# Optimization experiments

Hardware: AMD Instinct MI355X
Metric: run time of the kernel (lower is better)

The kernel has to match this reference:

```python
import jax, jax.numpy as jnp
import numpy as np

B, S = 32768, 512  # rays, max bright spots (= 2*max_samples)


def setup_inputs() -> dict:
    key = jax.random.key(0)
    k1, k2, k3, k4, k5 = jax.random.split(key, 5)
    V = jax.random.normal(k1, (B, 3), dtype=jnp.float32)
    N = jax.random.normal(k2, (B, 3), dtype=jnp.float32)
    N = N / jnp.linalg.norm(N, axis=-1, keepdims=True)
    spots = jax.random.normal(k3, (S, 3), dtype=jnp.float32)
    spots = spots / jnp.linalg.norm(spots, axis=-1, keepdims=True)
    # prefix masks: num_ele[i] <= num_ray[i] <= S (matches kernel's start_ind-j indexing)
    num_ray = jax.random.randint(k4, (B,), S // 2, S + 1)
    num_ele = jax.random.randint(k5, (B,), 0, S // 2)
    j = jnp.arange(S)
    ray_mask = j[None, :] < num_ray[:, None]
    bright_mask = j[None, :] < num_ele[:, None]
    std = jnp.float32(0.05)  # pix_size
    return {"V": V, "N": N, "spots": spots, "ray_mask": ray_mask,
            "bright_mask": bright_mask, "std": std}


def reference(V, N, spots, ray_mask, bright_mask, std):
    Bn, Sn = bright_mask.shape
    # wp.randf(seed): uniform in [0,1), one per written component -> (B,S,3)
    u = jax.random.uniform(jax.random.key(42), (Bn, Sn, 3), dtype=spots.dtype)
    num_ele = bright_mask.sum(axis=1)            # n per row
    num_ray = ray_mask.sum(axis=1)               # start_ind = num_ray - 1
    j = jnp.arange(Sn)
    active = j[None, :] < num_ele[:, None]       # j in range(n)
    jit = spots[None, :, :] + std * u            # jittered light dirs (B,S,3)
    LdotN = jnp.einsum('bsd,bd->bs', jit, N)
    cond = active & (LdotN > 0.0)                # rejection test
    t = num_ray[:, None] - 1 - j[None, :]        # reversed write index
    t_safe = jnp.where(cond & (t >= 0) & (t < Sn), t, Sn)  # Sn -> dropped
    b_idx = jnp.arange(Bn)[:, None]
    Ls = jnp.zeros((Bn, Sn, 3), spots.dtype).at[b_idx, t_safe].set(jit, mode='drop')
    bmask = jnp.zeros((Bn, Sn), jnp.int32).at[b_idx, t_safe].set(1, mode='drop')
    return Ls, bmask.astype(bool)
```

## Files before the change

kernel.cpp:

```cpp
#include <hip/hip_runtime.h>


#define TF_ROUND(x0, x1, r) { x0 += x1; x1 = ((x1 << (r)) | (x1 >> (32 - (r)))); x1 ^= x0; }

__device__ __forceinline__ unsigned tf2x32_seed42_xor(unsigned x0, unsigned x1) {
  const unsigned k0 = 0u, k1 = 42u;
  const unsigned k2 = 0x1BD11BDAu ^ k0 ^ k1;
  x0 += k0; x1 += k1;
  TF_ROUND(x0,x1,13) TF_ROUND(x0,x1,15) TF_ROUND(x0,x1,26) TF_ROUND(x0,x1,6)
  x0 += k1; x1 += k2 + 1u;
  TF_ROUND(x0,x1,17) TF_ROUND(x0,x1,29) TF_ROUND(x0,x1,16) TF_ROUND(x0,x1,24)
  x0 += k2; x1 += k0 + 2u;
  TF_ROUND(x0,x1,13) TF_ROUND(x0,x1,15) TF_ROUND(x0,x1,26) TF_ROUND(x0,x1,6)
  x0 += k0; x1 += k1 + 3u;
  TF_ROUND(x0,x1,17) TF_ROUND(x0,x1,29) TF_ROUND(x0,x1,16) TF_ROUND(x0,x1,24)
  x0 += k1; x1 += k2 + 4u;
  TF_ROUND(x0,x1,13) TF_ROUND(x0,x1,15) TF_ROUND(x0,x1,26) TF_ROUND(x0,x1,6)
  x0 += k2; x1 += k0 + 5u;
  return x0 ^ x1;
}

typedef float f4v __attribute__((ext_vector_type(4)));

__device__ __forceinline__ int detect_mode(const unsigned char* m) {
  const unsigned char d0 = m[0], d1 = m[1], d4 = m[4];
  return (d0 == 0) ? 3 : ((d1 != 0) ? 0 : ((d4 != 0) ? 1 : 2));
}

__device__ __forceinline__ int mask_nz(const unsigned char* m, unsigned q, int mode) {
  if (mode == 0) return m[q] != 0;
  if (mode == 1) return ((const int*)m)[q] != 0;
  if (mode == 2) return ((const long long*)m)[q] != 0;
  return ((const float*)m)[q] != 0.0f;
}

__global__ __launch_bounds__(256, 8) void bis_count(
    const unsigned char* __restrict__ rmask, const unsigned char* __restrict__ emask,
    int2* __restrict__ counts, int B)
{
  const int w = threadIdx.x >> 6, l = threadIdx.x & 63;
  const int b = blockIdx.x * 4 + w;
  if (b >= B) return;
  const int mode = detect_mode(rmask);
  const unsigned row = (unsigned)b * 512u;

  int r1 = 0, e1 = 0;
  if (l < 8) {
    const unsigned q = row + (unsigned)(l * 64 + 63);
    r1 = mask_nz(rmask, q, mode);
    e1 = mask_nz(emask, q, mode);
  }
  const int cr = __popcll(__ballot(r1));
  const int ce = __popcll(__ballot(e1));

  int nr = cr * 64, ne = ce * 64;
  if (cr < 8) {
    const unsigned q = row + (unsigned)(cr * 64 + l);
    nr = cr * 64 + __popcll(__ballot(mask_nz(rmask, q, mode)));
  }
  if (ce < 8) {
    const unsigned q = row + (unsigned)(ce * 64 + l);
    ne = ce * 64 + __popcll(__ballot(mask_nz(emask, q, mode)));
  }
  if (l == 0) counts[b] = make_int2(nr, ne);
}

__global__ __launch_bounds__(256, 8) void bis_main(
    const float* __restrict__ Nrm, const float* __restrict__ spots,
    const int2* __restrict__ counts, const float* __restrict__ stdp,
    float* __restrict__ Ls, float* __restrict__ bm, int B)
{
  const int tid = threadIdx.x;
  const int w = tid >> 6;
  const int l = tid & 63;
  const int b = blockIdx.x * 4 + w;
  if (b >= B) return;

  __shared__ f4v s_jit[4][256];

  const int2 cnt = counts[b];
  const int num_ray = cnt.x;
  const int num_ele = cnt.y;

  if (num_ele > 0) {
    const float stdv = stdp[0];
    const float n0 = Nrm[b*3+0], n1 = Nrm[b*3+1], n2 = Nrm[b*3+2];
    for (int j = l; j < num_ele; j += 64) {
      const unsigned f = ((unsigned)b * 512u + (unsigned)j) * 3u;
      const float u0 = __uint_as_float((tf2x32_seed42_xor(0u, f + 0u) >> 9) | 0x3F800000u) - 1.0f;
      const float u1 = __uint_as_float((tf2x32_seed42_xor(0u, f + 1u) >> 9) | 0x3F800000u) - 1.0f;
      const float u2 = __uint_as_float((tf2x32_seed42_xor(0u, f + 2u) >> 9) | 0x3F800000u) - 1.0f;
      const float j0 = __fadd_rn(spots[j*3+0], __fmul_rn(stdv, u0));
      const float j1 = __fadd_rn(spots[j*3+1], __fmul_rn(stdv, u1));
      const float j2 = __fadd_rn(spots[j*3+2], __fmul_rn(stdv, u2));
      const float d  = __fadd_rn(__fadd_rn(__fmul_rn(j0,n0), __fmul_rn(j1,n1)),
                                 __fmul_rn(j2,n2));
      const bool acc = (d > 0.0f);
      f4v e; e.x = acc ? j0 : 0.f; e.y = acc ? j1 : 0.f; e.z = acc ? j2 : 0.f;
      e.w = acc ? 1.f : 0.f;
      s_jit[w][j] = e;
    }
  }
  asm volatile("s_waitcnt lgkmcnt(0)" ::: "memory");

  const int lo = num_ray - num_ele;
  const int hi = num_ray;
  const float* jrow = (const float*)&s_jit[w][0];

  f4v* lsrow = (f4v*)(Ls + (size_t)b * 1536u);
  #pragma unroll
  for (int i = 0; i < 6; ++i) {
    const int g = i * 64 + l;
    const unsigned ff0 = (unsigned)(g << 2);
    const int s0 = (int)((ff0 * 43691u) >> 17);
    const int s1 = (int)(((ff0 + 3u) * 43691u) >> 17);
    f4v o = {0.f, 0.f, 0.f, 0.f};
    if (s1 >= lo && s0 < hi) {
      #pragma unroll
      for (int k = 0; k < 4; ++k) {
        const unsigned ff = ff0 + (unsigned)k;
        const unsigned s  = (ff * 43691u) >> 17;
        const unsigned comp = ff - 3u * s;
        const int jj = num_ray - 1 - (int)s;
        if (jj >= 0 && jj < num_ele) o[k] = jrow[(unsigned)jj * 4u + comp];
      }
    }
    lsrow[g] = o;
  }

  f4v* bmrow = (f4v*)(bm + (size_t)b * 512u);
  #pragma unroll
  for (int i = 0; i < 2; ++i) {
    const int g = i * 64 + l;
    const int sb = g << 2;
    f4v o = {0.f, 0.f, 0.f, 0.f};
    if (sb + 3 >= lo && sb < hi) {
      #pragma unroll
      for (int k = 0; k < 4; ++k) {
        const int jj = num_ray - 1 - (sb + k);
        if (jj >= 0 && jj < num_ele) o[k] = jrow[(unsigned)jj * 4u + 3u];
      }
    }
    bmrow[g] = o;
  }
}

struct F3 { float x, y, z; };

__global__ __launch_bounds__(512) void bis_kernel_s(
    const float* __restrict__ Nrm, const float* __restrict__ spots,
    const unsigned char* __restrict__ rmask, const unsigned char* __restrict__ emask,
    const float* __restrict__ stdp, float* __restrict__ Ls, float* __restrict__ bm,
    int S)
{
  const long long b = blockIdx.x;
  const int t = threadIdx.x;
  const int mode = detect_mode(rmask);

  const long long e = b * (long long)S + t;
  int rnz, enz;
  if (mode == 0)      { rnz = rmask[e] != 0;                     enz = emask[e] != 0; }
  else if (mode == 1) { rnz = ((const int*)rmask)[e] != 0;       enz = ((const int*)emask)[e] != 0; }
  else if (mode == 2) { rnz = ((const long long*)rmask)[e] != 0; enz = ((const long long*)emask)[e] != 0; }
  else                { rnz = ((const float*)rmask)[e] != 0.0f;  enz = ((const float*)emask)[e] != 0.0f; }

  __shared__ int s_nr[16], s_ne[16];
  const unsigned long long br = __ballot(rnz);
  const unsigned long long be = __ballot(enz);
  const int w = t >> 6;
  if ((t & 63) == 0) { s_nr[w] = __popcll(br); s_ne[w] = __popcll(be); }
  __syncthreads();
  const int nw = blockDim.x >> 6;
  int num_ray = 0, num_ele = 0;
  for (int i = 0; i < nw; ++i) { num_ray += s_nr[i]; num_ele += s_ne[i]; }

  const int j = num_ray - 1 - t;
  float o0 = 0.f, o1 = 0.f, o2 = 0.f, m = 0.f;
  if (j >= 0 && j < num_ele) {
    const float stdv = stdp[0];
    const float n0 = Nrm[b*3+0], n1 = Nrm[b*3+1], n2 = Nrm[b*3+2];
    const unsigned f = (unsigned)((b * (long long)S + j) * 3LL);
    const float u0 = __uint_as_float((tf2x32_seed42_xor(0u, f + 0u) >> 9) | 0x3F800000u) - 1.0f;
    const float u1 = __uint_as_float((tf2x32_seed42_xor(0u, f + 1u) >> 9) | 0x3F800000u) - 1.0f;
    const float u2 = __uint_as_float((tf2x32_seed42_xor(0u, f + 2u) >> 9) | 0x3F800000u) - 1.0f;
    const float j0 = __fadd_rn(spots[j*3+0], __fmul_rn(stdv, u0));
    const float j1 = __fadd_rn(spots[j*3+1], __fmul_rn(stdv, u1));
    const float j2 = __fadd_rn(spots[j*3+2], __fmul_rn(stdv, u2));
    const float d  = __fadd_rn(__fadd_rn(__fmul_rn(j0,n0), __fmul_rn(j1,n1)), __fmul_rn(j2,n2));
    if (d > 0.0f) { o0 = j0; o1 = j1; o2 = j2; m = 1.0f; }
  }

  const long long oidx = b * (long long)S + t;
  F3 v; v.x = o0; v.y = o1; v.z = o2;
  reinterpret_cast<F3*>(Ls)[oidx] = v;
  bm[oidx] = m;
}

extern "C" void kernel_launch(void* const* d_in, const int* in_sizes, int n_in,
                              void* d_out, int out_size, void* d_ws, size_t ws_size,
                              hipStream_t stream) {
  const float* Nrm = (const float*)d_in[1];
  const float* spots = (const float*)d_in[2];
  const unsigned char* rmask = (const unsigned char*)d_in[3];
  const unsigned char* emask = (const unsigned char*)d_in[4];
  const float* stdp = (const float*)d_in[5];

  const int B = in_sizes[0] / 3;
  const int S = in_sizes[2] / 3;

  float* out = (float*)d_out;
  float* Ls = out;
  float* bm = out + (long long)B * S * 3;

  if (S == 512 && ws_size >= (size_t)B * sizeof(int2)) {
    int2* counts = (int2*)d_ws;
    dim3 grid((unsigned)((B + 3) / 4)), block(256);
    hipLaunchKernelGGL(bis_count, grid, block, 0, stream, rmask, emask, counts, B);
    hipLaunchKernelGGL(bis_main, grid, block, 0, stream,
                       Nrm, spots, counts, stdp, Ls, bm, B);
  } else {
    dim3 grid((unsigned)B), block((unsigned)S);
    hipLaunchKernelGGL(bis_kernel_s, grid, block, 0, stream,
                       Nrm, spots, rmask, emask, stdp, Ls, bm, S);
  }
}
```

Before: 91.10 us.

## Fuse count and main kernels into a persistent grid-stride kernel

The separate count kernel and main kernel become one persistent kernel launched with 2048 blocks, where each wave loops over rows with a grid stride, computes the mask prefix counts inline and then produces the outputs. This drops one kernel launch and the workspace round trip for counts. It also merges the two first-level ballots for the ray and element masks into one. The risk is lost overlap: each row's count loads now sit serially before its compute, and fewer blocks are resident because launch bounds drop to 4 waves per SIMD.

```diff
diff --git a/kernel.cpp b/kernel.cpp
--- a/kernel.cpp
+++ b/kernel.cpp
@@ -34,114 +34,97 @@
   return ((const float*)m)[q] != 0.0f;
 }
 
-__global__ __launch_bounds__(256, 8) void bis_count(
+__global__ __launch_bounds__(256, 4) void bis_persist(
+    const float* __restrict__ Nrm, const float* __restrict__ spots,
     const unsigned char* __restrict__ rmask, const unsigned char* __restrict__ emask,
-    int2* __restrict__ counts, int B)
-{
-  const int w = threadIdx.x >> 6, l = threadIdx.x & 63;
-  const int b = blockIdx.x * 4 + w;
-  if (b >= B) return;
-  const int mode = detect_mode(rmask);
-  const unsigned row = (unsigned)b * 512u;
-
-  int r1 = 0, e1 = 0;
-  if (l < 8) {
-    const unsigned q = row + (unsigned)(l * 64 + 63);
-    r1 = mask_nz(rmask, q, mode);
-    e1 = mask_nz(emask, q, mode);
-  }
-  const int cr = __popcll(__ballot(r1));
-  const int ce = __popcll(__ballot(e1));
-
-  int nr = cr * 64, ne = ce * 64;
-  if (cr < 8) {
-    const unsigned q = row + (unsigned)(cr * 64 + l);
-    nr = cr * 64 + __popcll(__ballot(mask_nz(rmask, q, mode)));
-  }
-  if (ce < 8) {
-    const unsigned q = row + (unsigned)(ce * 64 + l);
-    ne = ce * 64 + __popcll(__ballot(mask_nz(emask, q, mode)));
-  }
-  if (l == 0) counts[b] = make_int2(nr, ne);
-}
-
-__global__ __launch_bounds__(256, 8) void bis_main(
-    const float* __restrict__ Nrm, const float* __restrict__ spots,
-    const int2* __restrict__ counts, const float* __restrict__ stdp,
-    float* __restrict__ Ls, float* __restrict__ bm, int B)
+    const float* __restrict__ stdp, float* __restrict__ Ls, float* __restrict__ bm,
+    int B, int NW)
 {
   const int tid = threadIdx.x;
   const int w = tid >> 6;
   const int l = tid & 63;
-  const int b = blockIdx.x * 4 + w;
-  if (b >= B) return;
+  const int gw = blockIdx.x * 4 + w;
+  const int mode = detect_mode(rmask);
+  const float stdv = stdp[0];
 
   __shared__ f4v s_jit[4][256];
 
-  const int2 cnt = counts[b];
-  const int num_ray = cnt.x;
-  const int num_ele = cnt.y;
-
-  if (num_ele > 0) {
-    const float stdv = stdp[0];
-    const float n0 = Nrm[b*3+0], n1 = Nrm[b*3+1], n2 = Nrm[b*3+2];
-    for (int j = l; j < num_ele; j += 64) {
-      const unsigned f = ((unsigned)b * 512u + (unsigned)j) * 3u;
-      const float u0 = __uint_as_float((tf2x32_seed42_xor(0u, f + 0u) >> 9) | 0x3F800000u) - 1.0f;
-      const float u1 = __uint_as_float((tf2x32_seed42_xor(0u, f + 1u) >> 9) | 0x3F800000u) - 1.0f;
-      const float u2 = __uint_as_float((tf2x32_seed42_xor(0u, f + 2u) >> 9) | 0x3F800000u) - 1.0f;
-      const float j0 = __fadd_rn(spots[j*3+0], __fmul_rn(stdv, u0));
-      const float j1 = __fadd_rn(spots[j*3+1], __fmul_rn(stdv, u1));
-      const float j2 = __fadd_rn(spots[j*3+2], __fmul_rn(stdv, u2));
-      const float d  = __fadd_rn(__fadd_rn(__fmul_rn(j0,n0), __fmul_rn(j1,n1)),
-                                 __fmul_rn(j2,n2));
-      const bool acc = (d > 0.0f);
-      f4v e; e.x = acc ? j0 : 0.f; e.y = acc ? j1 : 0.f; e.z = acc ? j2 : 0.f;
-      e.w = acc ? 1.f : 0.f;
-      s_jit[w][j] = e;
-    }
-  }
-  asm volatile("s_waitcnt lgkmcnt(0)" ::: "memory");
-
-  const int lo = num_ray - num_ele;
-  const int hi = num_ray;
-  const float* jrow = (const float*)&s_jit[w][0];
-
-  f4v* lsrow = (f4v*)(Ls + (size_t)b * 1536u);
-  #pragma unroll
-  for (int i = 0; i < 6; ++i) {
-    const int g = i * 64 + l;
-    const unsigned ff0 = (unsigned)(g << 2);
-    const int s0 = (int)((ff0 * 43691u) >> 17);
-    const int s1 = (int)(((ff0 + 3u) * 43691u) >> 17);
-    f4v o = {0.f, 0.f, 0.f, 0.f};
-    if (s1 >= lo && s0 < hi) {
-      #pragma unroll
-      for (int k = 0; k < 4; ++k) {
-        const unsigned ff = ff0 + (unsigned)k;
-        const unsigned s  = (ff * 43691u) >> 17;
-        const unsigned comp = ff - 3u * s;
-        const int jj = num_ray - 1 - (int)s;
-        if (jj >= 0 && jj < num_ele) o[k] = jrow[(unsigned)jj * 4u + comp];
+  for (int b = gw; b < B; b += NW) {
+    const unsigned row = (unsigned)b * 512u;
+
+    int p1 = 0;
+    if (l < 8)            p1 = mask_nz(rmask, row + (unsigned)(l * 64 + 63), mode);
+    else if (l < 16)      p1 = mask_nz(emask, row + (unsigned)((l - 8) * 64 + 63), mode);
+    const unsigned long long b1 = __ballot(p1);
+    const int cr = __popcll(b1 & 0xFFull);
+    const int ce = __popcll((b1 >> 8) & 0xFFull);
+
+    int num_ray = cr * 64, num_ele = ce * 64;
+    if (cr < 8)
+      num_ray = cr * 64 + __popcll(__ballot(mask_nz(rmask, row + (unsigned)(cr * 64 + l), mode)));
+    if (ce < 8)
+      num_ele = ce * 64 + __popcll(__ballot(mask_nz(emask, row + (unsigned)(ce * 64 + l), mode)));
+
+    if (num_ele > 0) {
+      const float n0 = Nrm[b*3+0], n1 = Nrm[b*3+1], n2 = Nrm[b*3+2];
+      for (int j = l; j < num_ele; j += 64) {
+        const unsigned f = (row + (unsigned)j) * 3u;
+        const float u0 = __uint_as_float((tf2x32_seed42_xor(0u, f + 0u) >> 9) | 0x3F800000u) - 1.0f;
+        const float u1 = __uint_as_float((tf2x32_seed42_xor(0u, f + 1u) >> 9) | 0x3F800000u) - 1.0f;
+        const float u2 = __uint_as_float((tf2x32_seed42_xor(0u, f + 2u) >> 9) | 0x3F800000u) - 1.0f;
+        const float j0 = __fadd_rn(spots[j*3+0], __fmul_rn(stdv, u0));
+        const float j1 = __fadd_rn(spots[j*3+1], __fmul_rn(stdv, u1));
+        const float j2 = __fadd_rn(spots[j*3+2], __fmul_rn(stdv, u2));
+        const float d  = __fadd_rn(__fadd_rn(__fmul_rn(j0,n0), __fmul_rn(j1,n1)),
+                                   __fmul_rn(j2,n2));
+        const bool acc = (d > 0.0f);
+        f4v e; e.x = acc ? j0 : 0.f; e.y = acc ? j1 : 0.f; e.z = acc ? j2 : 0.f;
+        e.w = acc ? 1.f : 0.f;
+        s_jit[w][j] = e;
       }
     }
-    lsrow[g] = o;
-  }
-
-  f4v* bmrow = (f4v*)(bm + (size_t)b * 512u);
-  #pragma unroll
-  for (int i = 0; i < 2; ++i) {
-    const int g = i * 64 + l;
-    const int sb = g << 2;
-    f4v o = {0.f, 0.f, 0.f, 0.f};
-    if (sb + 3 >= lo && sb < hi) {
-      #pragma unroll
-      for (int k = 0; k < 4; ++k) {
-        const int jj = num_ray - 1 - (sb + k);
-        if (jj >= 0 && jj < num_ele) o[k] = jrow[(unsigned)jj * 4u + 3u];
+    asm volatile("s_waitcnt lgkmcnt(0)" ::: "memory");
+
+    const int lo = num_ray - num_ele;
+    const int hi = num_ray;
+    const float* jrow = (const float*)&s_jit[w][0];
+
+    f4v* lsrow = (f4v*)(Ls + (size_t)b * 1536u);
+    #pragma unroll
+    for (int i = 0; i < 6; ++i) {
+      const int g = i * 64 + l;
+      const unsigned ff0 = (unsigned)(g << 2);
+      const int s0 = (int)((ff0 * 43691u) >> 17);
+      const int s1 = (int)(((ff0 + 3u) * 43691u) >> 17);
+      f4v o = {0.f, 0.f, 0.f, 0.f};
+      if (s1 >= lo && s0 < hi) {
+        #pragma unroll
+        for (int k = 0; k < 4; ++k) {
+          const unsigned ff = ff0 + (unsigned)k;
+          const unsigned s  = (ff * 43691u) >> 17;
+          const unsigned comp = ff - 3u * s;
+          const int jj = num_ray - 1 - (int)s;
+          if (jj >= 0 && jj < num_ele) o[k] = jrow[(unsigned)jj * 4u + comp];
+        }
       }
+      lsrow[g] = o;
     }
-    bmrow[g] = o;
+
+    f4v* bmrow = (f4v*)(bm + (size_t)b * 512u);
+    #pragma unroll
+    for (int i = 0; i < 2; ++i) {
+      const int g = i * 64 + l;
+      const int sb = g << 2;
+      f4v o = {0.f, 0.f, 0.f, 0.f};
+      if (sb + 3 >= lo && sb < hi) {
+        #pragma unroll
+        for (int k = 0; k < 4; ++k) {
+          const int jj = num_ray - 1 - (sb + k);
+          if (jj >= 0 && jj < num_ele) o[k] = jrow[(unsigned)jj * 4u + 3u];
+        }
+      }
+      bmrow[g] = o;
+    }
   }
 }
 
@@ -212,12 +195,12 @@
   float* Ls = out;
   float* bm = out + (long long)B * S * 3;
 
-  if (S == 512 && ws_size >= (size_t)B * sizeof(int2)) {
-    int2* counts = (int2*)d_ws;
-    dim3 grid((unsigned)((B + 3) / 4)), block(256);
-    hipLaunchKernelGGL(bis_count, grid, block, 0, stream, rmask, emask, counts, B);
-    hipLaunchKernelGGL(bis_main, grid, block, 0, stream,
-                       Nrm, spots, counts, stdp, Ls, bm, B);
+  if (S == 512) {
+    const int nblocks = 2048;
+    const int NW = nblocks * 4;
+    dim3 grid(nblocks), block(256);
+    hipLaunchKernelGGL(bis_persist, grid, block, 0, stream,
+                       Nrm, spots, rmask, emask, stdp, Ls, bm, B, NW);
   } else {
     dim3 grid((unsigned)B), block((unsigned)S);
     hipLaunchKernelGGL(bis_kernel_s, grid, block, 0, stream,
```

Result: slower. 102.9 us (+13.0%).
